# Kernel tuning notes

Hardware: AMD Instinct MI355X
Metric: run time of the kernel (lower is better)

## Reference

```python
import jax, jax.numpy as jnp
import numpy as np

IN_DIM, HID = 256, 10
B, H, W = 4, 128, 128
ADJ = np.array([
    [0,1,0,0,0,0],
    [1,0,1,1,1,1],
    [0,1,0,0,0,0],
    [0,1,0,0,0,0],
    [0,1,0,0,0,1],
    [0,1,0,0,1,0]], dtype=np.int32)
EDGES = np.argwhere(ADJ)                      # [E,2] rows = (src, dst), torch.nonzero order
SRC = jnp.asarray(EDGES[:, 0])
DST = jnp.asarray(EDGES[:, 1])
HALF_IDX = jnp.asarray([0, 0, 0, 0, 1, 1])    # parts 1-4 -> upper half, 5-6 -> lower half


def _grouped_att(x, Wg, bg):
    # grouped 1x1 conv (groups=n, one output channel per node) + sigmoid
    # x [n,B,h,H,W], Wg [n,h], bg [n] -> [n,B,1,H,W]
    return jax.nn.sigmoid(jnp.einsum('nbchw,nc->nbhw', x, Wg) + bg[:, None, None, None])[:, :, None]


def _composition(x, Wg, bg):
    # attention-gated sum of child node states -> message [B,h,H,W]
    return (_grouped_att(x, Wg, bg) * x).sum(0)


def _part_dependency(fea, x, Wf, Wx, b):
    # relu(conv1x1(cat([fea, x_i], ch))) per node; fea contribution computed once
    # fea [B,C,H,W], x [n,B,h,H,W] -> [n,B,h,H,W]
    f = jnp.einsum('bchw,oc->bohw', fea, Wf)
    return jax.nn.relu(f[None] + jnp.einsum('nbchw,oc->nbohw', x, Wx)
                       + b[None, None, :, None, None])


def _decomposition(fea, x_src, x_dst, Wf, Wx, b):
    # att = sigmoid(conv1x1(cat([fea, x_dst]))) with per-node weights; gates x_src
    att = jax.nn.sigmoid(jnp.einsum('bchw,nc->nbhw', fea, Wf)
                         + jnp.einsum('nbchw,nc->nbhw', x_dst, Wx)
                         + b[:, None, None, None])[:, :, None]
    return att * x_src


def _att_update(x, m, Wa, ba, Wu):
    # attention-gated fused update; x,m [n,B,h,H,W]; Wa [n,1,2h], Wu [n,h,2h]
    cat = jnp.concatenate([x, m], axis=2)
    att = jax.nn.sigmoid(jnp.einsum('nbchw,noc->nbohw', cat, Wa) + ba[:, None, :, None, None])
    upd = jax.nn.relu(jnp.einsum('nbchw,noc->nbohw', cat, Wu))
    return x * (1.0 - att) + upd * att


def _gnn(P):
    xp, xh, xf, p_fea, h_fea = P['xp'], P['xh'], P['xf'], P['p_fea'], P['h_fea']
    # ---------- Full graph ----------
    xf_msg = _composition(xh, P['Wf_comp'], P['bf_comp'])
    xf_new = _att_update(xf[None], xf_msg[None], P['Wf_uatt'], P['bf_uatt'], P['Wf_uupd'])
    # ---------- Half graph ----------
    h_dp = _part_dependency(h_fea, xh, P['Wh_pdp_f'], P['Wh_pdp_x'], P['bh_pdp'])  # [2,B,h,H,W]
    h_att = _grouped_att(xh, P['Wh_att'], P['bh_att'])                              # [2,B,1,H,W]
    xphu = _composition(xp[:4], P['Wh_cu'], P['bh_cu'])
    xphl = _composition(xp[4:], P['Wh_cl'], P['bh_cl'])
    xlh = h_dp[1] * h_att[1] * (1.0 - h_att[0])   # lower -> upper
    xuh = h_dp[0] * h_att[0] * (1.0 - h_att[1])   # upper -> lower
    xfh = _decomposition(h_fea, xf[None], xh, P['Wh_dec_f'], P['Wh_dec_x'], P['bh_dec'])
    h_msg = jnp.stack([xphu + xlh, xphl + xuh]) + xfh
    xh_new = _att_update(xh, h_msg, P['Wh_uatt'], P['bh_uatt'], P['Wh_uupd'])
    # ---------- Part graph: edge-wise gather + segment-sum scatter ----------
    p_dp = _part_dependency(p_fea, xp, P['Wp_pdp_f'], P['Wp_pdp_x'], P['bp_pdp'])  # [6,B,h,H,W]
    p_att = _grouped_att(xp, P['Wp_att'], P['bp_att'])                              # [6,B,1,H,W]
    e_msg = p_dp[SRC] * p_att[SRC] * (1.0 - p_att[DST])                             # [E,B,h,H,W]
    xpp = jax.ops.segment_sum(e_msg, DST, num_segments=6)
    xhp = _decomposition(p_fea, xh[HALF_IDX], xp, P['Wp_dec_f'], P['Wp_dec_x'], P['bp_dec'])
    xp_new = _att_update(xp, xpp + xhp, P['Wp_uatt'], P['bp_uatt'], P['Wp_uupd'])
    # stacked node states: 6 parts, 2 halves, 1 full -> [9,B,h,H,W]
    return jnp.concatenate([xp_new, xh_new, xf_new], axis=0)


def setup_inputs() -> dict:
    key = jax.random.key(0)
    ks = iter(jax.random.split(key, 64))
    def rnd(shape, s=1.0):
        return jax.random.normal(next(ks), shape, dtype=jnp.float32) * s
    return {
        'xp': rnd((6, B, HID, H, W)),
        'xh': rnd((2, B, HID, H, W)),
        'xf': rnd((B, HID, H, W)),
        'bg_node': rnd((B, HID, H, W)),
        'p_fea': rnd((B, IN_DIM, H, W)),
        'h_fea': rnd((B, IN_DIM, H, W)),
        'f_fea': rnd((B, IN_DIM, H, W)),
        'Wf_comp': rnd((2, HID), 0.3), 'bf_comp': rnd((2,), 0.1),
        'Wf_uatt': rnd((1, 1, 2 * HID), 0.3), 'bf_uatt': rnd((1, 1), 0.1),
        'Wf_uupd': rnd((1, HID, 2 * HID), 0.3),
        'Wh_pdp_f': rnd((HID, IN_DIM), 0.05), 'Wh_pdp_x': rnd((HID, HID), 0.3), 'bh_pdp': rnd((HID,), 0.1),
        'Wh_att': rnd((2, HID), 0.3), 'bh_att': rnd((2,), 0.1),
        'Wh_cu': rnd((4, HID), 0.3), 'bh_cu': rnd((4,), 0.1),
        'Wh_cl': rnd((2, HID), 0.3), 'bh_cl': rnd((2,), 0.1),
        'Wh_dec_f': rnd((2, IN_DIM), 0.05), 'Wh_dec_x': rnd((2, HID), 0.3), 'bh_dec': rnd((2,), 0.1),
        'Wh_uatt': rnd((2, 1, 2 * HID), 0.3), 'bh_uatt': rnd((2, 1), 0.1),
        'Wh_uupd': rnd((2, HID, 2 * HID), 0.3),
        'Wp_pdp_f': rnd((HID, IN_DIM), 0.05), 'Wp_pdp_x': rnd((HID, HID), 0.3), 'bp_pdp': rnd((HID,), 0.1),
        'Wp_att': rnd((6, HID), 0.3), 'bp_att': rnd((6,), 0.1),
        'Wp_dec_f': rnd((6, IN_DIM), 0.05), 'Wp_dec_x': rnd((6, HID), 0.3), 'bp_dec': rnd((6,), 0.1),
        'Wp_uatt': rnd((6, 1, 2 * HID), 0.3), 'bp_uatt': rnd((6, 1), 0.1),
        'Wp_uupd': rnd((6, HID, 2 * HID), 0.3),
    }


def reference(xp, xh, xf, bg_node, p_fea, h_fea, f_fea,
              Wf_comp, bf_comp, Wf_uatt, bf_uatt, Wf_uupd,
              Wh_pdp_f, Wh_pdp_x, bh_pdp, Wh_att, bh_att,
              Wh_cu, bh_cu, Wh_cl, bh_cl,
              Wh_dec_f, Wh_dec_x, bh_dec, Wh_uatt, bh_uatt, Wh_uupd,
              Wp_pdp_f, Wp_pdp_x, bp_pdp, Wp_att, bp_att,
              Wp_dec_f, Wp_dec_x, bp_dec, Wp_uatt, bp_uatt, Wp_uupd):
    P = dict(locals())
    return _gnn(P)
```

## Files before the change

### kernel.cpp

```cpp
#include <hip/hip_runtime.h>


namespace {
constexpr int S     = 128 * 128;
constexpr int BATCH = 4;
constexpr int HID   = 10;
constexpr int INDIM = 256;
constexpr int NPIX  = BATCH * S;

struct Ptrs {
  const float* __restrict__ xp;
  const float* __restrict__ xh;
  const float* __restrict__ xf;
  const float* __restrict__ p_fea;
  const float* __restrict__ h_fea;
  const float* __restrict__ Wf_comp;  const float* __restrict__ bf_comp;
  const float* __restrict__ Wf_uatt;  const float* __restrict__ bf_uatt;
  const float* __restrict__ Wf_uupd;
  const float* __restrict__ Wh_pdp_f; const float* __restrict__ Wh_pdp_x;
  const float* __restrict__ bh_pdp;
  const float* __restrict__ Wh_att;   const float* __restrict__ bh_att;
  const float* __restrict__ Wh_cu;    const float* __restrict__ bh_cu;
  const float* __restrict__ Wh_cl;    const float* __restrict__ bh_cl;
  const float* __restrict__ Wh_dec_f; const float* __restrict__ Wh_dec_x;
  const float* __restrict__ bh_dec;
  const float* __restrict__ Wh_uatt;  const float* __restrict__ bh_uatt;
  const float* __restrict__ Wh_uupd;
  const float* __restrict__ Wp_pdp_f; const float* __restrict__ Wp_pdp_x;
  const float* __restrict__ bp_pdp;
  const float* __restrict__ Wp_att;   const float* __restrict__ bp_att;
  const float* __restrict__ Wp_dec_f; const float* __restrict__ Wp_dec_x;
  const float* __restrict__ bp_dec;
  const float* __restrict__ Wp_uatt;  const float* __restrict__ bp_uatt;
  const float* __restrict__ Wp_uupd;
  float* __restrict__ out;
  float* __restrict__ ws;
};

__device__ __forceinline__ float sigmoidf(float x) {
  return 1.0f / (1.0f + __expf(-x));
}


constexpr int LROW = 65;

template <int NO>
__device__ __forceinline__ void proj_impl(
    float* lds,
    const float* __restrict__ fea,
    const float* __restrict__ Wa,
    const float* __restrict__ Wb,
    float* __restrict__ ws, int obase) {
  const int t   = threadIdx.x;
  const int pxg = t & 63;
  const int sl  = __builtin_amdgcn_readfirstlane(t >> 6);
  const int pb  = blockIdx.x * 256;
  const int b   = pb >> 14;
  const int p0  = pb & (S - 1);

  float4 acc[NO];
#pragma unroll
  for (int o = 0; o < NO; ++o) acc[o] = float4{0.f, 0.f, 0.f, 0.f};

  const float4* __restrict__ base =
      (const float4*)(fea + (size_t)(b * INDIM + sl * 64) * S + p0) + pxg;

  float4 cur[8];
#pragma unroll
  for (int i = 0; i < 8; ++i) cur[i] = base[(size_t)i * (S / 4)];

#pragma unroll
  for (int blk = 0; blk < 8; ++blk) {
    float4 nxt[8];
    if (blk < 7) {
#pragma unroll
      for (int i = 0; i < 8; ++i)
        nxt[i] = base[(size_t)((blk + 1) * 8 + i) * (S / 4)];
    }
#pragma unroll
    for (int i = 0; i < 8; ++i) {
      const int c = sl * 64 + blk * 8 + i;
      const float4 v = cur[i];
#pragma unroll
      for (int o = 0; o < 10; ++o) {
        const float w = Wa[o * INDIM + c];
        acc[o].x = fmaf(v.x, w, acc[o].x);
        acc[o].y = fmaf(v.y, w, acc[o].y);
        acc[o].z = fmaf(v.z, w, acc[o].z);
        acc[o].w = fmaf(v.w, w, acc[o].w);
      }
#pragma unroll
      for (int o = 10; o < NO; ++o) {
        const float w = Wb[(o - 10) * INDIM + c];
        acc[o].x = fmaf(v.x, w, acc[o].x);
        acc[o].y = fmaf(v.y, w, acc[o].y);
        acc[o].z = fmaf(v.z, w, acc[o].z);
        acc[o].w = fmaf(v.w, w, acc[o].w);
      }
    }
    if (blk < 7) {
#pragma unroll
      for (int i = 0; i < 8; ++i) cur[i] = nxt[i];
    }
  }

  float* row = lds + (sl * 64 + pxg) * LROW;
#pragma unroll
  for (int o = 0; o < NO; ++o) {
    row[4 * o + 0] = acc[o].x;
    row[4 * o + 1] = acc[o].y;
    row[4 * o + 2] = acc[o].z;
    row[4 * o + 3] = acc[o].w;
  }
  __syncthreads();

  constexpr int K = NO / 4;
  const int og = t >> 6;
#pragma unroll
  for (int k = 0; k < K; ++k) {
    const int o = og * K + k;
    float r[4] = {0.f, 0.f, 0.f, 0.f};
#pragma unroll
    for (int s2 = 0; s2 < 4; ++s2) {
      const float* rr = lds + (s2 * 64 + pxg) * LROW + 4 * o;
#pragma unroll
      for (int j = 0; j < 4; ++j) r[j] += rr[j];
    }
    float4 res; res.x = r[0]; res.y = r[1]; res.z = r[2]; res.w = r[3];
    *(float4*)(ws + (size_t)(obase + o) * NPIX + pb + pxg * 4) = res;
  }
}

__global__ __launch_bounds__(256, 2) void proj_kernel(Ptrs P) {
  __shared__ float lds[256 * LROW];
  if (blockIdx.y == 0) {
    proj_impl<12>(lds, P.h_fea, P.Wh_pdp_f, P.Wh_dec_f, P.ws, 0);
  } else {
    proj_impl<16>(lds, P.p_fea, P.Wp_pdp_f, P.Wp_dec_f, P.ws, 12);
  }
}


__device__ __forceinline__ void att_update_store(
    const float* x, const float* m,
    const float* __restrict__ Wa, float ba, const float* __restrict__ Wu,
    float* __restrict__ outp) {
  float a = ba;
#pragma unroll
  for (int c = 0; c < HID; ++c) a = fmaf(x[c], Wa[c], a);
#pragma unroll
  for (int c = 0; c < HID; ++c) a = fmaf(m[c], Wa[HID + c], a);
  a = sigmoidf(a);
#pragma unroll
  for (int o = 0; o < HID; ++o) {
    float u = 0.f;
#pragma unroll
    for (int c = 0; c < HID; ++c) u = fmaf(x[c], Wu[o * 2 * HID + c], u);
#pragma unroll
    for (int c = 0; c < HID; ++c) u = fmaf(m[c], Wu[o * 2 * HID + HID + c], u);
    u = fmaxf(u, 0.f);
    outp[(size_t)o * S] = x[o] * (1.f - a) + u * a;
  }
}

__device__ __forceinline__ void load10(float* dst, const float* __restrict__ src,
                                       int plane, int p) {
#pragma unroll
  for (int c = 0; c < HID; ++c)
    dst[c] = src[((size_t)plane * HID + c) * S + p];
}

__global__ __launch_bounds__(256) void gnn_node(Ptrs P) {
  const int tid = blockIdx.x * blockDim.x + threadIdx.x;
  const int b = tid >> 14;
  const int p = tid & (S - 1);
  const int y = blockIdx.y;

  if (y == 8) {
    float xh0[HID], xh1[HID], xfv[HID];
    load10(xh0, P.xh, 0 * BATCH + b, p);
    load10(xh1, P.xh, 1 * BATCH + b, p);
    load10(xfv, P.xf, b, p);
    float a0 = P.bf_comp[0], a1 = P.bf_comp[1];
#pragma unroll
    for (int c = 0; c < HID; ++c) {
      a0 = fmaf(xh0[c], P.Wf_comp[c], a0);
      a1 = fmaf(xh1[c], P.Wf_comp[HID + c], a1);
    }
    a0 = sigmoidf(a0); a1 = sigmoidf(a1);
    float msg[HID];
#pragma unroll
    for (int c = 0; c < HID; ++c) msg[c] = a0 * xh0[c] + a1 * xh1[c];
    att_update_store(xfv, msg, P.Wf_uatt, P.bf_uatt[0], P.Wf_uupd,
                     P.out + ((size_t)(8 * BATCH + b) * HID) * S + p);
  } else if (y >= 6) {
    const int h = y - 6;
    float xh_self[HID], xh_oth[HID], xfv[HID], fh[HID];
    load10(xh_self, P.xh, h * BATCH + b, p);
    load10(xh_oth,  P.xh, (1 - h) * BATCH + b, p);
    load10(xfv, P.xf, b, p);
#pragma unroll
    for (int o = 0; o < HID; ++o) fh[o] = P.ws[(size_t)o * NPIX + tid];
    const float hdec = P.ws[(size_t)(10 + h) * NPIX + tid];

    const int nsrc = h ? 2 : 4;
    const int sbase = h ? 4 : 0;
    const float* __restrict__ Wc = h ? P.Wh_cl : P.Wh_cu;
    const float* __restrict__ bc = h ? P.bh_cl : P.bh_cu;
    float comp[HID];
#pragma unroll
    for (int o = 0; o < HID; ++o) comp[o] = 0.f;
#pragma unroll
    for (int i = 0; i < 4; ++i) {
      if (i < nsrc) {
        float xpi[HID];
        load10(xpi, P.xp, (sbase + i) * BATCH + b, p);
        float s = bc[i];
#pragma unroll
        for (int c = 0; c < HID; ++c) s = fmaf(xpi[c], Wc[i * HID + c], s);
        s = sigmoidf(s);
#pragma unroll
        for (int c = 0; c < HID; ++c) comp[c] = fmaf(s, xpi[c], comp[c]);
      }
    }

    float a_self = P.bh_att[h], a_oth = P.bh_att[1 - h];
#pragma unroll
    for (int c = 0; c < HID; ++c) {
      a_self = fmaf(xh_self[c], P.Wh_att[h * HID + c], a_self);
      a_oth  = fmaf(xh_oth[c],  P.Wh_att[(1 - h) * HID + c], a_oth);
    }
    a_self = sigmoidf(a_self); a_oth = sigmoidf(a_oth);
    const float wg = a_oth * (1.f - a_self);

    float d = hdec + P.bh_dec[h];
#pragma unroll
    for (int c = 0; c < HID; ++c) d = fmaf(xh_self[c], P.Wh_dec_x[h * HID + c], d);
    d = sigmoidf(d);

    float m[HID];
#pragma unroll
    for (int o = 0; o < HID; ++o) {
      float dp = fh[o] + P.bh_pdp[o];
#pragma unroll
      for (int c = 0; c < HID; ++c) dp = fmaf(xh_oth[c], P.Wh_pdp_x[o * HID + c], dp);
      dp = fmaxf(dp, 0.f);
      m[o] = comp[o] + dp * wg + d * xfv[o];
    }
    att_update_store(xh_self, m, P.Wh_uatt + h * 2 * HID, P.bh_uatt[h],
                     P.Wh_uupd + h * HID * 2 * HID,
                     P.out + ((size_t)((6 + h) * BATCH + b) * HID) * S + p);
  } else {
    const int n = y;
    const int half = (n < 4) ? 0 : 1;
    const unsigned masks[6] = {0x02u, 0x3Du, 0x02u, 0x02u, 0x22u, 0x12u};
    const unsigned mask = masks[n];

    float xpn[HID], xh_s[HID], fpj[HID];
    load10(xpn, P.xp, n * BATCH + b, p);
    load10(xh_s, P.xh, half * BATCH + b, p);
#pragma unroll
    for (int o = 0; o < HID; ++o) fpj[o] = P.ws[(size_t)(12 + o) * NPIX + tid];
    const float pdecn = P.ws[(size_t)(22 + n) * NPIX + tid];

    float pattn = P.bp_att[n];
#pragma unroll
    for (int c = 0; c < HID; ++c) pattn = fmaf(xpn[c], P.Wp_att[n * HID + c], pattn);
    pattn = sigmoidf(pattn);

    float msum[HID];
#pragma unroll
    for (int o = 0; o < HID; ++o) msum[o] = 0.f;
#pragma unroll
    for (int src = 0; src < 6; ++src) {
      if (mask & (1u << src)) {
        float xps[HID];
        load10(xps, P.xp, src * BATCH + b, p);
        float ps = P.bp_att[src];
#pragma unroll
        for (int c = 0; c < HID; ++c) ps = fmaf(xps[c], P.Wp_att[src * HID + c], ps);
        ps = sigmoidf(ps);
#pragma unroll
        for (int o = 0; o < HID; ++o) {
          float dp = fpj[o] + P.bp_pdp[o];
#pragma unroll
          for (int c = 0; c < HID; ++c) dp = fmaf(xps[c], P.Wp_pdp_x[o * HID + c], dp);
          msum[o] = fmaf(fmaxf(dp, 0.f), ps, msum[o]);
        }
      }
    }

    float dg = pdecn + P.bp_dec[n];
#pragma unroll
    for (int c = 0; c < HID; ++c) dg = fmaf(xpn[c], P.Wp_dec_x[n * HID + c], dg);
    dg = sigmoidf(dg);

    const float onem = 1.f - pattn;
    float m[HID];
#pragma unroll
    for (int o = 0; o < HID; ++o) m[o] = onem * msum[o] + dg * xh_s[o];

    att_update_store(xpn, m, P.Wp_uatt + n * 2 * HID, P.bp_uatt[n],
                     P.Wp_uupd + n * HID * 2 * HID,
                     P.out + ((size_t)(n * BATCH + b) * HID) * S + p);
  }
}

}

extern "C" void kernel_launch(void* const* d_in, const int* in_sizes, int n_in,
                              void* d_out, int out_size, void* d_ws, size_t ws_size,
                              hipStream_t stream) {
  Ptrs P;
  P.xp       = (const float*)d_in[0];
  P.xh       = (const float*)d_in[1];
  P.xf       = (const float*)d_in[2];
  P.p_fea    = (const float*)d_in[4];
  P.h_fea    = (const float*)d_in[5];
  P.Wf_comp  = (const float*)d_in[7];
  P.bf_comp  = (const float*)d_in[8];
  P.Wf_uatt  = (const float*)d_in[9];
  P.bf_uatt  = (const float*)d_in[10];
  P.Wf_uupd  = (const float*)d_in[11];
  P.Wh_pdp_f = (const float*)d_in[12];
  P.Wh_pdp_x = (const float*)d_in[13];
  P.bh_pdp   = (const float*)d_in[14];
  P.Wh_att   = (const float*)d_in[15];
  P.bh_att   = (const float*)d_in[16];
  P.Wh_cu    = (const float*)d_in[17];
  P.bh_cu    = (const float*)d_in[18];
  P.Wh_cl    = (const float*)d_in[19];
  P.bh_cl    = (const float*)d_in[20];
  P.Wh_dec_f = (const float*)d_in[21];
  P.Wh_dec_x = (const float*)d_in[22];
  P.bh_dec   = (const float*)d_in[23];
  P.Wh_uatt  = (const float*)d_in[24];
  P.bh_uatt  = (const float*)d_in[25];
  P.Wh_uupd  = (const float*)d_in[26];
  P.Wp_pdp_f = (const float*)d_in[27];
  P.Wp_pdp_x = (const float*)d_in[28];
  P.bp_pdp   = (const float*)d_in[29];
  P.Wp_att   = (const float*)d_in[30];
  P.bp_att   = (const float*)d_in[31];
  P.Wp_dec_f = (const float*)d_in[32];
  P.Wp_dec_x = (const float*)d_in[33];
  P.bp_dec   = (const float*)d_in[34];
  P.Wp_uatt  = (const float*)d_in[35];
  P.bp_uatt  = (const float*)d_in[36];
  P.Wp_uupd  = (const float*)d_in[37];
  P.out      = (float*)d_out;
  P.ws       = (float*)d_ws;

  proj_kernel<<<dim3(NPIX / 256, 2), dim3(256), 0, stream>>>(P);
  gnn_node<<<dim3(NPIX / 256, 9), dim3(256), 0, stream>>>(P);
}
```

Measured before the change: 70.72 us.

## Use one pixel per thread in projection kernel to raise occupancy

The channel-projection kernel now has each thread handle a single pixel with scalar loads instead of four pixels with float4 loads. The block covers 64 pixels instead of 256, the grid grows fourfold, and the LDS reduction buffer shrinks. Launch bounds rise to 8 blocks per CU. The aim is to cut register and LDS pressure so more waves hide memory latency, at the cost of narrower memory transactions and four times as many weight loads per pixel.

```diff
diff --git a/kernel.cpp b/kernel.cpp
--- a/kernel.cpp
+++ b/kernel.cpp
@@ -42,7 +42,7 @@
 }
 
 
-constexpr int LROW = 65;
+constexpr int LPAD = 17;
 
 template <int NO>
 __device__ __forceinline__ void proj_impl(
@@ -51,52 +51,41 @@
     const float* __restrict__ Wa,
     const float* __restrict__ Wb,
     float* __restrict__ ws, int obase) {
-  const int t   = threadIdx.x;
-  const int pxg = t & 63;
-  const int sl  = __builtin_amdgcn_readfirstlane(t >> 6);
-  const int pb  = blockIdx.x * 256;
-  const int b   = pb >> 14;
-  const int p0  = pb & (S - 1);
-
-  float4 acc[NO];
-#pragma unroll
-  for (int o = 0; o < NO; ++o) acc[o] = float4{0.f, 0.f, 0.f, 0.f};
-
-  const float4* __restrict__ base =
-      (const float4*)(fea + (size_t)(b * INDIM + sl * 64) * S + p0) + pxg;
-
-  float4 cur[8];
-#pragma unroll
-  for (int i = 0; i < 8; ++i) cur[i] = base[(size_t)i * (S / 4)];
+  const int t  = threadIdx.x;
+  const int px = t & 63;
+  const int sl = __builtin_amdgcn_readfirstlane(t >> 6);
+  const int pb = blockIdx.x * 64;
+  const int b  = pb >> 14;
+  const int p  = (pb & (S - 1)) + px;
+
+  float acc[NO];
+#pragma unroll
+  for (int o = 0; o < NO; ++o) acc[o] = 0.f;
+
+  const float* __restrict__ base = fea + (size_t)(b * INDIM + sl * 64) * S + p;
+
+  float cur[8];
+#pragma unroll
+  for (int i = 0; i < 8; ++i) cur[i] = base[(size_t)i * S];
 
 #pragma unroll
   for (int blk = 0; blk < 8; ++blk) {
-    float4 nxt[8];
+    float nxt[8];
     if (blk < 7) {
 #pragma unroll
       for (int i = 0; i < 8; ++i)
-        nxt[i] = base[(size_t)((blk + 1) * 8 + i) * (S / 4)];
+        nxt[i] = base[(size_t)((blk + 1) * 8 + i) * S];
     }
 #pragma unroll
     for (int i = 0; i < 8; ++i) {
       const int c = sl * 64 + blk * 8 + i;
-      const float4 v = cur[i];
-#pragma unroll
-      for (int o = 0; o < 10; ++o) {
-        const float w = Wa[o * INDIM + c];
-        acc[o].x = fmaf(v.x, w, acc[o].x);
-        acc[o].y = fmaf(v.y, w, acc[o].y);
-        acc[o].z = fmaf(v.z, w, acc[o].z);
-        acc[o].w = fmaf(v.w, w, acc[o].w);
-      }
-#pragma unroll
-      for (int o = 10; o < NO; ++o) {
-        const float w = Wb[(o - 10) * INDIM + c];
-        acc[o].x = fmaf(v.x, w, acc[o].x);
-        acc[o].y = fmaf(v.y, w, acc[o].y);
-        acc[o].z = fmaf(v.z, w, acc[o].z);
-        acc[o].w = fmaf(v.w, w, acc[o].w);
-      }
+      const float v = cur[i];
+#pragma unroll
+      for (int o = 0; o < 10; ++o)
+        acc[o] = fmaf(v, Wa[o * INDIM + c], acc[o]);
+#pragma unroll
+      for (int o = 10; o < NO; ++o)
+        acc[o] = fmaf(v, Wb[(o - 10) * INDIM + c], acc[o]);
     }
     if (blk < 7) {
 #pragma unroll
@@ -104,14 +93,9 @@
     }
   }
 
-  float* row = lds + (sl * 64 + pxg) * LROW;
-#pragma unroll
-  for (int o = 0; o < NO; ++o) {
-    row[4 * o + 0] = acc[o].x;
-    row[4 * o + 1] = acc[o].y;
-    row[4 * o + 2] = acc[o].z;
-    row[4 * o + 3] = acc[o].w;
-  }
+  float* row = lds + (sl * 64 + px) * LPAD;
+#pragma unroll
+  for (int o = 0; o < NO; ++o) row[o] = acc[o];
   __syncthreads();
 
   constexpr int K = NO / 4;
@@ -119,20 +103,16 @@
 #pragma unroll
   for (int k = 0; k < K; ++k) {
     const int o = og * K + k;
-    float r[4] = {0.f, 0.f, 0.f, 0.f};
-#pragma unroll
-    for (int s2 = 0; s2 < 4; ++s2) {
-      const float* rr = lds + (s2 * 64 + pxg) * LROW + 4 * o;
-#pragma unroll
-      for (int j = 0; j < 4; ++j) r[j] += rr[j];
-    }
-    float4 res; res.x = r[0]; res.y = r[1]; res.z = r[2]; res.w = r[3];
-    *(float4*)(ws + (size_t)(obase + o) * NPIX + pb + pxg * 4) = res;
-  }
-}
-
-__global__ __launch_bounds__(256, 2) void proj_kernel(Ptrs P) {
-  __shared__ float lds[256 * LROW];
+    const float s = lds[(0 * 64 + px) * LPAD + o] +
+                    lds[(1 * 64 + px) * LPAD + o] +
+                    lds[(2 * 64 + px) * LPAD + o] +
+                    lds[(3 * 64 + px) * LPAD + o];
+    ws[(size_t)(obase + o) * NPIX + pb + px] = s;
+  }
+}
+
+__global__ __launch_bounds__(256, 8) void proj_kernel(Ptrs P) {
+  __shared__ float lds[4 * 64 * LPAD];
   if (blockIdx.y == 0) {
     proj_impl<12>(lds, P.h_fea, P.Wh_pdp_f, P.Wh_dec_f, P.ws, 0);
   } else {
@@ -351,6 +331,6 @@
   P.out      = (float*)d_out;
   P.ws       = (float*)d_ws;
 
-  proj_kernel<<<dim3(NPIX / 256, 2), dim3(256), 0, stream>>>(P);
+  proj_kernel<<<dim3(NPIX / 64, 2), dim3(256), 0, stream>>>(P);
   gnn_node<<<dim3(NPIX / 256, 9), dim3(256), 0, stream>>>(P);
 }
```

After: 131.9 us. 86.5% more time.

## Stage projection weights in LDS and hand-pipeline feature loads with inline asm

Applied to the files above, without the earlier changes.

Rewrites the 256-channel projection kernel. Weights are staged into LDS in channel-major order and read as float4 vectors instead of scalar global loads. Feature loads are issued with inline global_load_dwordx4 into a rotating 8-deep buffer, using explicit vmcnt waits to keep loads in flight. The cross-wave reduction now runs in two passes with a smaller LDS stride to cut LDS usage. The inline asm and hand-placed waits add fragility and depend on the compiler respecting the scheduling barriers.

```diff
diff --git a/kernel.cpp b/kernel.cpp
--- a/kernel.cpp
+++ b/kernel.cpp
@@ -7,6 +7,14 @@
 constexpr int HID   = 10;
 constexpr int INDIM = 256;
 constexpr int NPIX  = BATCH * S;
+
+typedef float f32x4 __attribute__((ext_vector_type(4)));
+
+constexpr unsigned CHB  = S * 4;
+constexpr int WOFF      = 0;
+constexpr int ROFF      = 4096;
+constexpr int RSTR      = 33;
+constexpr int LDS_FLOATS = ROFF + 256 * RSTR;
 
 struct Ptrs {
   const float* __restrict__ xp;
@@ -42,7 +50,11 @@
 }
 
 
-constexpr int LROW = 65;
+#define ISSUE(i)                                                        \
+  asm volatile("global_load_dwordx4 %0, %1, %2"                        \
+               : "=&v"(r[i]) : "v"(voff[i]), "s"(sbase) : "memory")
+#define WAIT7  do { asm volatile("s_waitcnt vmcnt(7)" ::: "memory");    \
+                    __builtin_amdgcn_sched_barrier(0); } while (0)
 
 template <int NO>
 __device__ __forceinline__ void proj_impl(
@@ -58,81 +70,105 @@
   const int b   = pb >> 14;
   const int p0  = pb & (S - 1);
 
-  float4 acc[NO];
-#pragma unroll
-  for (int o = 0; o < NO; ++o) acc[o] = float4{0.f, 0.f, 0.f, 0.f};
-
-  const float4* __restrict__ base =
-      (const float4*)(fea + (size_t)(b * INDIM + sl * 64) * S + p0) + pxg;
-
-  float4 cur[8];
-#pragma unroll
-  for (int i = 0; i < 8; ++i) cur[i] = base[(size_t)i * (S / 4)];
-
-#pragma unroll
-  for (int blk = 0; blk < 8; ++blk) {
-    float4 nxt[8];
-    if (blk < 7) {
-#pragma unroll
-      for (int i = 0; i < 8; ++i)
-        nxt[i] = base[(size_t)((blk + 1) * 8 + i) * (S / 4)];
-    }
+  float* lds_w = lds + WOFF;
+  for (int i = t; i < NO * INDIM; i += 256) {
+    const int o = i >> 8, ch = i & 255;
+    const float wv = (o < 10) ? Wa[o * INDIM + ch] : Wb[(o - 10) * INDIM + ch];
+    lds_w[ch * NO + o] = wv;
+  }
+  __syncthreads();
+
+  f32x4 acc[NO];
+#pragma unroll
+  for (int o = 0; o < NO; ++o) acc[o] = (f32x4){0.f, 0.f, 0.f, 0.f};
+
+  const uint64_t sbase =
+      (uint64_t)(fea + (size_t)(b * INDIM + sl * 64) * S + p0);
+
+  f32x4    r[8];
+  unsigned voff[8];
+#pragma unroll
+  for (int i = 0; i < 8; ++i) {
+    voff[i] = (unsigned)i * CHB + (unsigned)(pxg * 16);
+    ISSUE(i);
+  }
+
+#pragma unroll 1
+  for (int blk = 0; blk < 7; ++blk) {
 #pragma unroll
     for (int i = 0; i < 8; ++i) {
-      const int c = sl * 64 + blk * 8 + i;
-      const float4 v = cur[i];
-#pragma unroll
-      for (int o = 0; o < 10; ++o) {
-        const float w = Wa[o * INDIM + c];
-        acc[o].x = fmaf(v.x, w, acc[o].x);
-        acc[o].y = fmaf(v.y, w, acc[o].y);
-        acc[o].z = fmaf(v.z, w, acc[o].z);
-        acc[o].w = fmaf(v.w, w, acc[o].w);
+      WAIT7;
+      const f32x4 v = r[i];
+      const int ch = blk * 8 + i;
+      const float* wrow = lds_w + (size_t)(sl * 64 + ch) * NO;
+#pragma unroll
+      for (int g = 0; g < NO / 4; ++g) {
+        const f32x4 w4 = *(const f32x4*)(wrow + 4 * g);
+        acc[4 * g + 0] += v * w4.x;
+        acc[4 * g + 1] += v * w4.y;
+        acc[4 * g + 2] += v * w4.z;
+        acc[4 * g + 3] += v * w4.w;
       }
-#pragma unroll
-      for (int o = 10; o < NO; ++o) {
-        const float w = Wb[(o - 10) * INDIM + c];
-        acc[o].x = fmaf(v.x, w, acc[o].x);
-        acc[o].y = fmaf(v.y, w, acc[o].y);
-        acc[o].z = fmaf(v.z, w, acc[o].z);
-        acc[o].w = fmaf(v.w, w, acc[o].w);
+      voff[i] += 8u * CHB;
+      ISSUE(i);
+    }
+  }
+#pragma unroll
+  for (int i = 0; i < 8; ++i) {
+    if      (i == 0) asm volatile("s_waitcnt vmcnt(7)" ::: "memory");
+    else if (i == 1) asm volatile("s_waitcnt vmcnt(6)" ::: "memory");
+    else if (i == 2) asm volatile("s_waitcnt vmcnt(5)" ::: "memory");
+    else if (i == 3) asm volatile("s_waitcnt vmcnt(4)" ::: "memory");
+    else if (i == 4) asm volatile("s_waitcnt vmcnt(3)" ::: "memory");
+    else if (i == 5) asm volatile("s_waitcnt vmcnt(2)" ::: "memory");
+    else if (i == 6) asm volatile("s_waitcnt vmcnt(1)" ::: "memory");
+    else             asm volatile("s_waitcnt vmcnt(0)" ::: "memory");
+    __builtin_amdgcn_sched_barrier(0);
+    const f32x4 v = r[i];
+    const int ch = 56 + i;
+    const float* wrow = lds_w + (size_t)(sl * 64 + ch) * NO;
+#pragma unroll
+    for (int g = 0; g < NO / 4; ++g) {
+      const f32x4 w4 = *(const f32x4*)(wrow + 4 * g);
+      acc[4 * g + 0] += v * w4.x;
+      acc[4 * g + 1] += v * w4.y;
+      acc[4 * g + 2] += v * w4.z;
+      acc[4 * g + 3] += v * w4.w;
+    }
+  }
+
+  float* red = lds + ROFF;
+  const int og = t >> 6;
+#pragma unroll 1
+  for (int pass = 0; pass < 2; ++pass) {
+    const int o0 = pass * 8;
+    const int NP = (pass == 0) ? 8 : (NO - 8);
+    __syncthreads();
+    float* row = red + (sl * 64 + pxg) * RSTR;
+    for (int k = 0; k < NP; ++k) {
+      const f32x4 a = acc[o0 + k];
+      row[4 * k + 0] = a.x; row[4 * k + 1] = a.y;
+      row[4 * k + 2] = a.z; row[4 * k + 3] = a.w;
+    }
+    __syncthreads();
+    const int K = NP / 4;
+    for (int k = 0; k < K; ++k) {
+      const int lo = og * K + k;
+      float rsum[4] = {0.f, 0.f, 0.f, 0.f};
+#pragma unroll
+      for (int s2 = 0; s2 < 4; ++s2) {
+        const float* rp = red + (s2 * 64 + pxg) * RSTR + 4 * lo;
+#pragma unroll
+        for (int j = 0; j < 4; ++j) rsum[j] += rp[j];
       }
-    }
-    if (blk < 7) {
-#pragma unroll
-      for (int i = 0; i < 8; ++i) cur[i] = nxt[i];
-    }
-  }
-
-  float* row = lds + (sl * 64 + pxg) * LROW;
-#pragma unroll
-  for (int o = 0; o < NO; ++o) {
-    row[4 * o + 0] = acc[o].x;
-    row[4 * o + 1] = acc[o].y;
-    row[4 * o + 2] = acc[o].z;
-    row[4 * o + 3] = acc[o].w;
-  }
-  __syncthreads();
-
-  constexpr int K = NO / 4;
-  const int og = t >> 6;
-#pragma unroll
-  for (int k = 0; k < K; ++k) {
-    const int o = og * K + k;
-    float r[4] = {0.f, 0.f, 0.f, 0.f};
-#pragma unroll
-    for (int s2 = 0; s2 < 4; ++s2) {
-      const float* rr = lds + (s2 * 64 + pxg) * LROW + 4 * o;
-#pragma unroll
-      for (int j = 0; j < 4; ++j) r[j] += rr[j];
-    }
-    float4 res; res.x = r[0]; res.y = r[1]; res.z = r[2]; res.w = r[3];
-    *(float4*)(ws + (size_t)(obase + o) * NPIX + pb + pxg * 4) = res;
+      float4 res; res.x = rsum[0]; res.y = rsum[1]; res.z = rsum[2]; res.w = rsum[3];
+      *(float4*)(ws + (size_t)(obase + o0 + lo) * NPIX + pb + pxg * 4) = res;
+    }
   }
 }
 
 __global__ __launch_bounds__(256, 2) void proj_kernel(Ptrs P) {
-  __shared__ float lds[256 * LROW];
+  __shared__ float lds[LDS_FLOATS];
   if (blockIdx.y == 0) {
     proj_impl<12>(lds, P.h_fea, P.Wh_pdp_f, P.Wh_dec_f, P.ws, 0);
   } else {
@@ -204,7 +240,7 @@
     const float hdec = P.ws[(size_t)(10 + h) * NPIX + tid];
 
     const int nsrc = h ? 2 : 4;
-    const int sbase = h ? 4 : 0;
+    const int sbase2 = h ? 4 : 0;
     const float* __restrict__ Wc = h ? P.Wh_cl : P.Wh_cu;
     const float* __restrict__ bc = h ? P.bh_cl : P.bh_cu;
     float comp[HID];
@@ -214,7 +250,7 @@
     for (int i = 0; i < 4; ++i) {
       if (i < nsrc) {
         float xpi[HID];
-        load10(xpi, P.xp, (sbase + i) * BATCH + b, p);
+        load10(xpi, P.xp, (sbase2 + i) * BATCH + b, p);
         float s = bc[i];
 #pragma unroll
         for (int c = 0; c < HID; ++c) s = fmaf(xpi[c], Wc[i * HID + c], s);
```

Result: no change. 70.33 us (-0.5%).
